# Kernel optimization log

Hardware: AMD Instinct MI355X
Metric: run time of the kernel (lower is better)

## Reference

```python
import jax, jax.numpy as jnp
import numpy as np

B, S, D = 32, 1024, 256
K, H, L = 64, 4, 4
KH, DV = K // H, D // H  # pooling key size per head, pooling value size
EPS = 1e-5
SCALE = 1.0 / np.sqrt(K).astype(np.float32)  # both encoder and pooling use sqrt(1/key_size)


def _ln(x, gamma=None, beta=None):
    m = jnp.mean(x, axis=-1, keepdims=True)
    v = jnp.mean(jnp.square(x - m), axis=-1, keepdims=True)
    y = (x - m) * jax.lax.rsqrt(v + EPS)
    if gamma is not None:
        y = y * gamma + beta
    return y


def setup_inputs() -> dict:
    key = jax.random.key(0)
    ks = iter(jax.random.split(key, 32))

    def w(shape, fan_in):
        return jax.random.normal(next(ks), shape, jnp.float32) / np.sqrt(fan_in).astype(np.float32)

    inp = {
        "input": jax.random.normal(next(ks), (B, S, D), jnp.float32),
        "lin0_W": w((D, D), D), "lin0_b": jnp.zeros((D,), jnp.float32),
        # stacked params for the 4 AttentionEncoder layers
        "enc_Wk": w((L, D, K), D), "enc_bk": jnp.zeros((L, K), jnp.float32),
        "enc_Wq": w((L, D, K), D), "enc_bq": jnp.zeros((L, K), jnp.float32),
        "enc_Wv": w((L, D, D), D), "enc_bv": jnp.zeros((L, D), jnp.float32),
        "enc_Wb": w((L, D, 1), D), "enc_bb": jnp.zeros((L, 1), jnp.float32),
        "enc_Wff": w((L, D, D), D), "enc_bff": jnp.zeros((L, D), jnp.float32),
        "enc_g1": jnp.ones((L, D), jnp.float32), "enc_beta1": jnp.zeros((L, D), jnp.float32),
        # multi-head pooling head
        "pool_Wk": w((D, KH), D), "pool_bk": jnp.zeros((KH,), jnp.float32),
        "pool_Wv": w((D, DV), D), "pool_bv": jnp.zeros((DV,), jnp.float32),
        "queries": jax.random.normal(next(ks), (H, KH), jnp.float32),
        "lin1_W": w((D, 2), D), "lin1_b": jnp.zeros((2,), jnp.float32),
    }
    return inp


def reference(input, lin0_W, lin0_b, enc_Wk, enc_bk, enc_Wq, enc_bq, enc_Wv, enc_bv,
              enc_Wb, enc_bb, enc_Wff, enc_bff, enc_g1, enc_beta1,
              pool_Wk, pool_bk, pool_Wv, pool_bv, queries, lin1_W, lin1_b):
    # NOTE: original code computes act0(lin0(input)) and then discards it (dead code);
    # it is omitted here since it does not affect the output.
    x = input
    for i in range(L):
        k = (x @ enc_Wk[i] + enc_bk[i]) * SCALE          # [B,S,K]
        q = x @ enc_Wq[i] + enc_bq[i]                     # [B,S,K]
        v = x @ enc_Wv[i] + enc_bv[i]                     # [B,S,D]
        bias = x @ enc_Wb[i] + enc_bb[i]                  # [B,S,1], broadcast over columns
        scores = jax.nn.sigmoid(jnp.einsum('bik,bjk->bij', k, q) + bias)  # [B,S,S]
        attn = jnp.einsum('bij,bjd->bid', scores, v)      # [B,S,D]
        res = _ln(x + attn, enc_g1[i], enc_beta1[i])
        ff = jax.nn.relu(res @ enc_Wff[i] + enc_bff[i])
        x = _ln(res + ff)                                 # norm2: no affine
    # multi-head pooling with learned queries
    pk = (x @ pool_Wk + pool_bk) * SCALE                  # [B,S,KH]
    pv = x @ pool_Wv + pool_bv                            # [B,S,DV]
    sc = jnp.einsum('bsk,hk->bsh', pk, queries)           # [B,S,H]
    sc = jax.nn.softmax(sc, axis=1)                       # softmax over sequence
    pooled = jnp.einsum('bsh,bsd->bhd', sc, pv).reshape(x.shape[0], -1)  # [B, H*DV]=[B,D]
    return pooled @ lin1_W + lin1_b                       # [B,2]
```

## Files before the change

### kernel.cpp

```cpp
#include <hip/hip_runtime.h>
#include <hip/hip_bf16.h>
#include <math.h>

#define BB 32
#define SS 1024
#define DD 256
#define MM (BB*SS)
#define LEPS 1e-5f

typedef __bf16 bf16x8 __attribute__((ext_vector_type(8)));
typedef __bf16 bf16x4 __attribute__((ext_vector_type(4)));
typedef float f32x4 __attribute__((ext_vector_type(4)));

__global__ __launch_bounds__(256) void cast_wt(const float* __restrict__ W,
                                               __bf16* __restrict__ WT,
                                               int N, float scale, int dstride, int noff) {
    int n = blockIdx.x, l = blockIdx.z, k = threadIdx.x;
    WT[(size_t)dstride * l + (size_t)(n + noff) * 256 + k] =
        (__bf16)(W[(size_t)256 * N * l + (size_t)k * N + n] * scale);
}

__global__ __launch_bounds__(128) void bias_combine(const float* __restrict__ bk,
                                                    const float* __restrict__ bq,
                                                    float* __restrict__ dst) {
    int l = blockIdx.x, j = threadIdx.x;
    dst[l * 128 + j] = (j < 64) ? bk[l * 64 + j] * 0.125f : bq[l * 64 + (j - 64)];
}

__global__ __launch_bounds__(256) void cast_x(const float* __restrict__ x, __bf16* __restrict__ xb) {
    size_t i = ((size_t)blockIdx.x * 256 + threadIdx.x) * 8;
    float4 a = *(const float4*)(x + i);
    float4 b = *(const float4*)(x + i + 4);
    __bf16 o[8] __attribute__((aligned(16)));
    o[0] = (__bf16)a.x; o[1] = (__bf16)a.y; o[2] = (__bf16)a.z; o[3] = (__bf16)a.w;
    o[4] = (__bf16)b.x; o[5] = (__bf16)b.y; o[6] = (__bf16)b.z; o[7] = (__bf16)b.w;
    *(bf16x8*)(xb + i) = *(bf16x8*)o;
}

template <int BN, int MODE>
__global__ __launch_bounds__(256) void gemm_mfma(const __bf16* __restrict__ A,
                                                 const __bf16* __restrict__ WT,
                                                 const float* __restrict__ bias,
                                                 float bscale, int relu,
                                                 void* __restrict__ Cv, void* __restrict__ Cv2,
                                                 int N) {
    constexpr int MR = (BN == 128) ? 4 : 2;
    constexpr int NC = (BN == 128) ? 4 : BN / 16;
    const int t = threadIdx.x;
    const int w = t >> 6, lane = t & 63;
    const int m0 = blockIdx.x * 128;
    const int n0 = blockIdx.y * BN;
    const size_t wt_z = (MODE == 3) ? (size_t)blockIdx.z * SS * 256 : 0;
    const size_t c_z  = (MODE == 3) ? (size_t)blockIdx.z * 256 * (size_t)N : 0;
    const int wr = (BN == 128) ? (w >> 1) * 64 : w * 32;
    const int wc = (BN == 128) ? (w & 1) * 64 : 0;
    __shared__ __align__(16) __bf16 smem[128 * 64 + BN * 64];
    __bf16 (*Al)[64] = (__bf16(*)[64])smem;
    __bf16 (*Wl)[64] = (__bf16(*)[64])(smem + 128 * 64);
    f32x4 acc[MR][NC] = {};

    for (int k0 = 0; k0 < 256; k0 += 64) {
        __syncthreads();
        {
            int r = t >> 1, half = t & 1;
            const __bf16* src = A + (size_t)(m0 + r) * 256 + k0 + half * 32;
            bf16x8 v0 = *(const bf16x8*)(src);
            bf16x8 v1 = *(const bf16x8*)(src + 8);
            bf16x8 v2 = *(const bf16x8*)(src + 16);
            bf16x8 v3 = *(const bf16x8*)(src + 24);
            int cb = half * 4;
            *(bf16x8*)&Al[r][((cb + 0) ^ (r & 7)) * 8] = v0;
            *(bf16x8*)&Al[r][((cb + 1) ^ (r & 7)) * 8] = v1;
            *(bf16x8*)&Al[r][((cb + 2) ^ (r & 7)) * 8] = v2;
            *(bf16x8*)&Al[r][((cb + 3) ^ (r & 7)) * 8] = v3;
        }
        if (BN == 128) {
            int r = t >> 1, half = t & 1;
            const __bf16* src = WT + wt_z + (size_t)(n0 + r) * 256 + k0 + half * 32;
            bf16x8 v0 = *(const bf16x8*)(src);
            bf16x8 v1 = *(const bf16x8*)(src + 8);
            bf16x8 v2 = *(const bf16x8*)(src + 16);
            bf16x8 v3 = *(const bf16x8*)(src + 24);
            int cb = half * 4;
            *(bf16x8*)&Wl[r][((cb + 0) ^ (r & 7)) * 8] = v0;
            *(bf16x8*)&Wl[r][((cb + 1) ^ (r & 7)) * 8] = v1;
            *(bf16x8*)&Wl[r][((cb + 2) ^ (r & 7)) * 8] = v2;
            *(bf16x8*)&Wl[r][((cb + 3) ^ (r & 7)) * 8] = v3;
        } else if (BN == 64) {
            int n = t >> 2, q = t & 3;
            const __bf16* src = WT + (size_t)(n0 + n) * 256 + k0 + q * 16;
            bf16x8 v0 = *(const bf16x8*)src;
            bf16x8 v1 = *(const bf16x8*)(src + 8);
            *(bf16x8*)&Wl[n][((q * 2 + 0) ^ (n & 7)) * 8] = v0;
            *(bf16x8*)&Wl[n][((q * 2 + 1) ^ (n & 7)) * 8] = v1;
        } else {
            if (t < 128) {
                int n = t >> 3, c = t & 7;
                bf16x8 v = *(const bf16x8*)(WT + (size_t)(n0 + n) * 256 + k0 + c * 8);
                *(bf16x8*)&Wl[n][(c ^ (n & 7)) * 8] = v;
            }
        }
        __syncthreads();
#pragma unroll
        for (int ks = 0; ks < 2; ks++) {
            int c = ks * 4 + (lane >> 4);
            bf16x8 af[MR];
#pragma unroll
            for (int mf = 0; mf < MR; mf++) {
                int i = wr + mf * 16 + (lane & 15);
                af[mf] = *(const bf16x8*)&Al[i][(c ^ (i & 7)) * 8];
            }
#pragma unroll
            for (int nf = 0; nf < NC; nf++) {
                int n = wc + nf * 16 + (lane & 15);
                bf16x8 bfr = *(const bf16x8*)&Wl[n][(c ^ (n & 7)) * 8];
#pragma unroll
                for (int mf = 0; mf < MR; mf++)
                    acc[mf][nf] = __builtin_amdgcn_mfma_f32_16x16x32_bf16(af[mf], bfr, acc[mf][nf], 0, 0, 0);
            }
        }
    }
    if (MODE == 3) {
        __syncthreads();
#pragma unroll
        for (int mf = 0; mf < MR; mf++) {
#pragma unroll
            for (int nf = 0; nf < NC; nf++) {
                int col = wc + nf * 16 + (lane & 15);
#pragma unroll
                for (int r = 0; r < 4; r++) {
                    int row = wr + mf * 16 + (lane >> 4) * 4 + r;
                    float v = acc[mf][nf][r] + bias[m0 + row];
                    smem[row * 128 + (((col >> 3) ^ (row & 15)) * 8) + (col & 7)] = (__bf16)v;
                }
            }
        }
        __syncthreads();
#pragma unroll
        for (int p = 0; p < 2; p++) {
            int row = p * 64 + (t >> 2);
            int cq = (t & 3) * 4;
            __bf16* dst = (__bf16*)Cv + c_z + (size_t)(m0 + row) * N + n0 + (t & 3) * 32;
#pragma unroll
            for (int u = 0; u < 4; u++) {
                int ch = (cq + u) ^ (row & 15);
                *(bf16x8*)(dst + u * 8) = *(const bf16x8*)&smem[row * 128 + ch * 8];
            }
        }
        return;
    }
#pragma unroll
    for (int mf = 0; mf < MR; mf++) {
#pragma unroll
        for (int nf = 0; nf < NC; nf++) {
            int col = n0 + wc + nf * 16 + (lane & 15);
            float bcol = bias[col] * bscale;
#pragma unroll
            for (int r = 0; r < 4; r++) {
                int row = m0 + wr + mf * 16 + (lane >> 4) * 4 + r;
                float v = acc[mf][nf][r] + bcol;
                if (relu) v = fmaxf(v, 0.f);
                if (MODE == 2) {
                    if (col < 64) ((__bf16*)Cv)[(size_t)row * 64 + col] = (__bf16)v;
                    else ((__bf16*)Cv2)[(size_t)row * 64 + (col - 64)] = (__bf16)v;
                } else if (MODE == 1) {
                    ((__bf16*)Cv)[(size_t)row * N + col] = (__bf16)v;
                } else {
                    ((float*)Cv)[(size_t)row * N + col] = v;
                }
            }
        }
    }
}

__global__ __launch_bounds__(256) void bias_gemv(const __bf16* __restrict__ X,
                                                 const float* __restrict__ Wb,
                                                 const float* __restrict__ bb,
                                                 float* __restrict__ out) {
    int wave = threadIdx.x >> 6, lane = threadIdx.x & 63;
    size_t row = (size_t)blockIdx.x * 4 + wave;
    bf16x4 xv = *(const bf16x4*)(X + row * 256 + lane * 4);
    float4 wv = *(const float4*)(Wb + lane * 4);
    float p = (float)xv[0] * wv.x + (float)xv[1] * wv.y + (float)xv[2] * wv.z + (float)xv[3] * wv.w;
    for (int off = 32; off; off >>= 1) p += __shfl_down(p, off, 64);
    if (lane == 0) out[row] = p + bb[0];
}

__global__ __launch_bounds__(512, 4) void attn_mfma(const __bf16* __restrict__ kb,
                                                    const __bf16* __restrict__ qb,
                                                    const __bf16* __restrict__ vT,
                                                    const float* __restrict__ biasb,
                                                    const __bf16* __restrict__ xinb,
                                                    const float* __restrict__ gamma,
                                                    const float* __restrict__ beta,
                                                    __bf16* __restrict__ outb) {
    int h = blockIdx.x;
    int blow = h & 7, rest = h >> 3;
    int ib = rest & 15;
    int b = blow + (rest >> 4) * 8;
    const int i0 = ib * 64;
    const int t = threadIdx.x;
    const int w = t >> 6, lane = t & 63;
    const int iq = w >> 1;
    const int dhalf = w & 1;

    __shared__ __align__(16) __bf16 Kl[64][64];
    __shared__ __align__(16) __bf16 Ql[64][64];
    __shared__ __align__(16) __bf16 Vl[256][64];
    __shared__ __align__(16) __bf16 Sl[64][64];
    __shared__ float bsh[64];
    __shared__ float rowred[2][64][2];

    const int qj = t >> 3, qc = t & 7;
    const __bf16* qsrc_base = qb + ((size_t)(b * SS + qj)) * 64 + qc * 8;
    const int vd = t >> 1, vjh = t & 1;
    const __bf16* vsrc_base = vT + ((size_t)b * 256 + vd) * SS + vjh * 32;

    {
        int i = t >> 3, c = t & 7;
        bf16x8 v = *(const bf16x8*)(kb + ((size_t)(b * SS + i0 + i)) * 64 + c * 8);
        *(bf16x8*)&Kl[i][(c ^ (i & 7)) * 8] = v;
        if (t < 64) bsh[t] = biasb[b * SS + i0 + t];
    }
    {
        bf16x8 qv = *(const bf16x8*)(qsrc_base);
        *(bf16x8*)&Ql[qj][(qc ^ (qj & 7)) * 8] = qv;
#pragma unroll
        for (int u = 0; u < 4; u++) {
            bf16x8 v = *(const bf16x8*)(vsrc_base + u * 8);
            *(bf16x8*)&Vl[vd][((vjh * 4 + u) ^ (vd & 7)) * 8] = v;
        }
    }
    __syncthreads();

    f32x4 acc[8] = {};

    for (int j0 = 0; j0 < SS; j0 += 64) {
        const bool has_next = (j0 + 64) < SS;
        bf16x8 qn;
        bf16x8 vn0, vn1, vn2, vn3;
        if (has_next) {
            qn = *(const bf16x8*)(qsrc_base + (size_t)(j0 + 64) * 64);
            const __bf16* vs = vsrc_base + j0 + 64;
            vn0 = *(const bf16x8*)(vs);
            vn1 = *(const bf16x8*)(vs + 8);
            vn2 = *(const bf16x8*)(vs + 16);
            vn3 = *(const bf16x8*)(vs + 24);
        }
#pragma unroll
        for (int jj = 0; jj < 2; jj++) {
            int jq = (w & 1) * 2 + jj;
            f32x4 sacc = {0.f, 0.f, 0.f, 0.f};
            __builtin_amdgcn_s_setprio(1);
#pragma unroll
            for (int ks = 0; ks < 2; ks++) {
                int i = iq * 16 + (lane & 15);
                int ck = ks * 4 + (lane >> 4);
                bf16x8 a = *(const bf16x8*)&Kl[i][(ck ^ (i & 7)) * 8];
                int j = jq * 16 + (lane & 15);
                bf16x8 bq = *(const bf16x8*)&Ql[j][(ck ^ (j & 7)) * 8];
                sacc = __builtin_amdgcn_mfma_f32_16x16x32_bf16(a, bq, sacc, 0, 0, 0);
            }
            __builtin_amdgcn_s_setprio(0);
            int jcol = jq * 16 + (lane & 15);
#pragma unroll
            for (int r = 0; r < 4; r++) {
                int irow = iq * 16 + (lane >> 4) * 4 + r;
                float x = sacc[r] + bsh[irow];
                float sg = 1.f / (1.f + __expf(-x));
                Sl[irow][(((jcol >> 3) ^ (irow & 7)) * 8) + (jcol & 7)] = (__bf16)sg;
            }
        }
        __syncthreads();
        bf16x8 am[2];
#pragma unroll
        for (int m = 0; m < 2; m++) {
            int i = iq * 16 + (lane & 15);
            int cj = m * 4 + (lane >> 4);
            am[m] = *(const bf16x8*)&Sl[i][(cj ^ (i & 7)) * 8];
        }
        __builtin_amdgcn_s_setprio(1);
#pragma unroll
        for (int dq = 0; dq < 8; dq++) {
            int d = dhalf * 128 + dq * 16 + (lane & 15);
#pragma unroll
            for (int m = 0; m < 2; m++) {
                int cj = m * 4 + (lane >> 4);
                bf16x8 bv = *(const bf16x8*)&Vl[d][(cj ^ (d & 7)) * 8];
                acc[dq] = __builtin_amdgcn_mfma_f32_16x16x32_bf16(am[m], bv, acc[dq], 0, 0, 0);
            }
        }
        __builtin_amdgcn_s_setprio(0);
        __syncthreads();
        if (has_next) {
            *(bf16x8*)&Ql[qj][(qc ^ (qj & 7)) * 8] = qn;
            *(bf16x8*)&Vl[vd][((vjh * 4 + 0) ^ (vd & 7)) * 8] = vn0;
            *(bf16x8*)&Vl[vd][((vjh * 4 + 1) ^ (vd & 7)) * 8] = vn1;
            *(bf16x8*)&Vl[vd][((vjh * 4 + 2) ^ (vd & 7)) * 8] = vn2;
            *(bf16x8*)&Vl[vd][((vjh * 4 + 3) ^ (vd & 7)) * 8] = vn3;
            __syncthreads();
        }
    }

#pragma unroll
    for (int r = 0; r < 4; r++) {
        int il = iq * 16 + (lane >> 4) * 4 + r;
        size_t rowoff = ((size_t)(b * SS + i0 + il)) * 256 + dhalf * 128 + (lane & 15);
#pragma unroll
        for (int dq = 0; dq < 8; dq++)
            acc[dq][r] += (float)xinb[rowoff + dq * 16];
    }
    float sr[4], qr[4];
#pragma unroll
    for (int r = 0; r < 4; r++) {
        float s = 0.f, q = 0.f;
#pragma unroll
        for (int dq = 0; dq < 8; dq++) {
            float v = acc[dq][r];
            s += v; q += v * v;
        }
#pragma unroll
        for (int mask = 8; mask; mask >>= 1) {
            s += __shfl_xor(s, mask, 64);
            q += __shfl_xor(q, mask, 64);
        }
        sr[r] = s; qr[r] = q;
    }
    if ((lane & 15) == 0) {
#pragma unroll
        for (int r = 0; r < 4; r++) {
            int il = iq * 16 + (lane >> 4) * 4 + r;
            rowred[dhalf][il][0] = sr[r];
            rowred[dhalf][il][1] = qr[r];
        }
    }
    __syncthreads();
    float gv[8], bv2[8];
#pragma unroll
    for (int dq = 0; dq < 8; dq++) {
        int d = dhalf * 128 + dq * 16 + (lane & 15);
        gv[dq] = gamma[d];
        bv2[dq] = beta[d];
    }
#pragma unroll
    for (int r = 0; r < 4; r++) {
        int il = iq * 16 + (lane >> 4) * 4 + r;
        float st = rowred[0][il][0] + rowred[1][il][0];
        float qt = rowred[0][il][1] + rowred[1][il][1];
        float mean = st * (1.f / 256.f);
        float var = qt * (1.f / 256.f) - mean * mean;
        float inv = 1.f / sqrtf(var + LEPS);
        size_t rowoff = ((size_t)(b * SS + i0 + il)) * 256 + dhalf * 128 + (lane & 15);
#pragma unroll
        for (int dq = 0; dq < 8; dq++) {
            float o = (acc[dq][r] - mean) * inv * gv[dq] + bv2[dq];
            outb[rowoff + dq * 16] = (__bf16)o;
        }
    }
}

__global__ __launch_bounds__(512) void gemm_ff_ln2(const __bf16* __restrict__ A,
                                                   const __bf16* __restrict__ WT,
                                                   const float* __restrict__ bias,
                                                   const __bf16* __restrict__ resid,
                                                   __bf16* __restrict__ outb) {
    const int t = threadIdx.x;
    const int w = t >> 6, lane = t & 63;
    const int m0 = blockIdx.x * 128;
    const int wr = (w >> 2) * 64, wc = (w & 3) * 64;
    __shared__ __align__(16) __bf16 Al[128][64];
    __shared__ __align__(16) __bf16 Wl[256][64];
    __shared__ float rowred[4][128][2];
    f32x4 acc[4][4] = {};

    for (int k0 = 0; k0 < 256; k0 += 64) {
        __syncthreads();
        {
            int r = t >> 2, c0 = (t & 3) * 2;
            const __bf16* src = A + (size_t)(m0 + r) * 256 + k0 + c0 * 8;
            bf16x8 v0 = *(const bf16x8*)src;
            bf16x8 v1 = *(const bf16x8*)(src + 8);
            *(bf16x8*)&Al[r][((c0 + 0) ^ (r & 7)) * 8] = v0;
            *(bf16x8*)&Al[r][((c0 + 1) ^ (r & 7)) * 8] = v1;
        }
        {
            int n = t >> 1, c0 = (t & 1) * 4;
            const __bf16* src = WT + (size_t)n * 256 + k0 + c0 * 8;
#pragma unroll
            for (int u = 0; u < 4; u++) {
                bf16x8 v = *(const bf16x8*)(src + u * 8);
                *(bf16x8*)&Wl[n][((c0 + u) ^ (n & 7)) * 8] = v;
            }
        }
        __syncthreads();
#pragma unroll
        for (int ks = 0; ks < 2; ks++) {
            int c = ks * 4 + (lane >> 4);
            bf16x8 af[4];
#pragma unroll
            for (int mf = 0; mf < 4; mf++) {
                int i = wr + mf * 16 + (lane & 15);
                af[mf] = *(const bf16x8*)&Al[i][(c ^ (i & 7)) * 8];
            }
#pragma unroll
            for (int nf = 0; nf < 4; nf++) {
                int n = wc + nf * 16 + (lane & 15);
                bf16x8 bfr = *(const bf16x8*)&Wl[n][(c ^ (n & 7)) * 8];
#pragma unroll
                for (int mf = 0; mf < 4; mf++)
                    acc[mf][nf] = __builtin_amdgcn_mfma_f32_16x16x32_bf16(af[mf], bfr, acc[mf][nf], 0, 0, 0);
            }
        }
    }
    float colb[4];
#pragma unroll
    for (int nf = 0; nf < 4; nf++) colb[nf] = bias[wc + nf * 16 + (lane & 15)];
#pragma unroll
    for (int mf = 0; mf < 4; mf++) {
#pragma unroll
        for (int r = 0; r < 4; r++) {
            int rl = wr + mf * 16 + (lane >> 4) * 4 + r;
            const __bf16* rrow = resid + (size_t)(m0 + rl) * 256 + wc + (lane & 15);
            float s = 0.f, q = 0.f;
#pragma unroll
            for (int nf = 0; nf < 4; nf++) {
                float v = fmaxf(acc[mf][nf][r] + colb[nf], 0.f) + (float)rrow[nf * 16];
                acc[mf][nf][r] = v;
                s += v; q += v * v;
            }
#pragma unroll
            for (int msk = 1; msk <= 8; msk <<= 1) {
                s += __shfl_xor(s, msk, 64);
                q += __shfl_xor(q, msk, 64);
            }
            if ((lane & 15) == 0) {
                rowred[w & 3][rl][0] = s;
                rowred[w & 3][rl][1] = q;
            }
        }
    }
    __syncthreads();
#pragma unroll
    for (int mf = 0; mf < 4; mf++) {
#pragma unroll
        for (int r = 0; r < 4; r++) {
            int rl = wr + mf * 16 + (lane >> 4) * 4 + r;
            float s = rowred[0][rl][0] + rowred[1][rl][0] + rowred[2][rl][0] + rowred[3][rl][0];
            float q = rowred[0][rl][1] + rowred[1][rl][1] + rowred[2][rl][1] + rowred[3][rl][1];
            float mean = s * (1.f / 256.f);
            float var = q * (1.f / 256.f) - mean * mean;
            float inv = 1.f / sqrtf(var + LEPS);
            size_t base = (size_t)(m0 + rl) * 256 + wc + (lane & 15);
#pragma unroll
            for (int nf = 0; nf < 4; nf++) {
                float o = (acc[mf][nf][r] - mean) * inv;
                outb[base + nf * 16] = (__bf16)o;
            }
        }
    }
}

__global__ __launch_bounds__(256) void pool_softmax(const float* __restrict__ pk,
                                                    const float* __restrict__ queries,
                                                    float* __restrict__ wout) {
    const int b = blockIdx.x, h = blockIdx.y;
    const int t = threadIdx.x;
    const int wv = t >> 6, lane = t & 63;
    __shared__ float qv[16];
    __shared__ float redm[4], reds[4];
    if (t < 16) qv[t] = queries[h * 16 + t];
    __syncthreads();
    float sc[4];
#pragma unroll
    for (int c = 0; c < 4; c++) {
        int s = c * 256 + t;
        const float* p = pk + ((size_t)b * SS + s) * 16;
        float4 a0 = *(const float4*)p;
        float4 a1 = *(const float4*)(p + 4);
        float4 a2 = *(const float4*)(p + 8);
        float4 a3 = *(const float4*)(p + 12);
        sc[c] = a0.x * qv[0] + a0.y * qv[1] + a0.z * qv[2] + a0.w * qv[3]
              + a1.x * qv[4] + a1.y * qv[5] + a1.z * qv[6] + a1.w * qv[7]
              + a2.x * qv[8] + a2.y * qv[9] + a2.z * qv[10] + a2.w * qv[11]
              + a3.x * qv[12] + a3.y * qv[13] + a3.z * qv[14] + a3.w * qv[15];
    }
    float m = fmaxf(fmaxf(sc[0], sc[1]), fmaxf(sc[2], sc[3]));
    for (int off = 32; off; off >>= 1) m = fmaxf(m, __shfl_xor(m, off, 64));
    if (lane == 0) redm[wv] = m;
    __syncthreads();
    m = fmaxf(fmaxf(redm[0], redm[1]), fmaxf(redm[2], redm[3]));
    float e[4];
    float sum = 0.f;
#pragma unroll
    for (int c = 0; c < 4; c++) { e[c] = expf(sc[c] - m); sum += e[c]; }
    for (int off = 32; off; off >>= 1) sum += __shfl_xor(sum, off, 64);
    if (lane == 0) reds[wv] = sum;
    __syncthreads();
    float inv = 1.f / (reds[0] + reds[1] + reds[2] + reds[3]);
#pragma unroll
    for (int c = 0; c < 4; c++)
        wout[((size_t)(b * 4 + h)) * SS + c * 256 + t] = e[c] * inv;
}

__global__ __launch_bounds__(256) void pool_wsum(const float* __restrict__ wgt,
                                                 const float* __restrict__ pv,
                                                 float* __restrict__ partial) {
    const int b = blockIdx.x, c = blockIdx.y;
    const int h = threadIdx.x >> 6, d = threadIdx.x & 63;
    const float* wrow = wgt + ((size_t)(b * 4 + h)) * SS + c * 64;
    const float* pvb = pv + ((size_t)(b * SS + c * 64)) * 64 + d;
    float a = 0.f;
#pragma unroll 8
    for (int s = 0; s < 64; s++) a += wrow[s] * pvb[(size_t)s * 64];
    partial[((size_t)b * 16 + c) * 256 + threadIdx.x] = a;
}

__global__ __launch_bounds__(256) void pool_final(const float* __restrict__ partial,
                                                  const float* __restrict__ W1,
                                                  const float* __restrict__ b1,
                                                  float* __restrict__ out) {
    const int b = blockIdx.x, t = threadIdx.x;
    __shared__ float r0[256], r1[256];
    float a = 0.f;
#pragma unroll
    for (int c = 0; c < 16; c++) a += partial[((size_t)b * 16 + c) * 256 + t];
    r0[t] = a * W1[t * 2 + 0];
    r1[t] = a * W1[t * 2 + 1];
    __syncthreads();
    for (int off = 128; off > 0; off >>= 1) {
        if (t < off) { r0[t] += r0[t + off]; r1[t] += r1[t + off]; }
        __syncthreads();
    }
    if (t == 0) {
        out[b * 2 + 0] = r0[0] + b1[0];
        out[b * 2 + 1] = r1[0] + b1[1];
    }
}

extern "C" void kernel_launch(void* const* d_in, const int* in_sizes, int n_in,
                              void* d_out, int out_size, void* d_ws, size_t ws_size,
                              hipStream_t stream) {
    const float* input = (const float*)d_in[0];
    const float* eWk = (const float*)d_in[3];
    const float* ebk = (const float*)d_in[4];
    const float* eWq = (const float*)d_in[5];
    const float* ebq = (const float*)d_in[6];
    const float* eWv = (const float*)d_in[7];
    const float* ebv = (const float*)d_in[8];
    const float* eWb = (const float*)d_in[9];
    const float* ebb = (const float*)d_in[10];
    const float* eWff = (const float*)d_in[11];
    const float* ebff = (const float*)d_in[12];
    const float* eg1 = (const float*)d_in[13];
    const float* ebe1 = (const float*)d_in[14];
    const float* pWk = (const float*)d_in[15];
    const float* pbk = (const float*)d_in[16];
    const float* pWv = (const float*)d_in[17];
    const float* pbv = (const float*)d_in[18];
    const float* qrs = (const float*)d_in[19];
    const float* W1 = (const float*)d_in[20];
    const float* b1 = (const float*)d_in[21];
    float* out = (float*)d_out;

    float* ws = (float*)d_ws;
    float* xbuf = ws;
    __bf16* xbf = (__bf16*)(xbuf + (size_t)MM * DD);
    float* tmp2 = (float*)(xbf + (size_t)MM * DD);
    float* r3 = tmp2 + (size_t)MM * DD;
    __bf16* tmp2bf = (__bf16*)r3;
    __bf16* vTb = tmp2bf + (size_t)MM * DD;
    float* r4 = r3 + (size_t)MM * DD;
    __bf16* kbf = (__bf16*)r4;
    __bf16* qbf = kbf + (size_t)MM * 64;
    float* bbuf = r4 + (size_t)MM * (DD / 2);
    __bf16* wbf = (__bf16*)(bbuf + MM);

    __bf16* WkqT = wbf;
    __bf16* WvT = WkqT + 4 * 128 * 256;
    __bf16* WffT = WvT + 4 * 256 * 256;
    __bf16* pWkT = WffT + 4 * 256 * 256;
    __bf16* pWvT = pWkT + 16 * 256;
    float* biasc = (float*)(pWvT + 64 * 256);

    float* pkbuf = tmp2;
    float* pvbuf = tmp2 + (size_t)MM * 16;
    float* wgtbuf = tmp2 + (size_t)MM * 80;
    float* partial = wgtbuf + (size_t)BB * 4 * SS;

    const float SC = 0.125f;

    cast_wt<<<dim3(64, 1, 4), 256, 0, stream>>>(eWk, WkqT, 64, SC, 128 * 256, 0);
    cast_wt<<<dim3(64, 1, 4), 256, 0, stream>>>(eWq, WkqT, 64, 1.f, 128 * 256, 64);
    cast_wt<<<dim3(256, 1, 4), 256, 0, stream>>>(eWv, WvT, 256, 1.f, 256 * 256, 0);
    cast_wt<<<dim3(256, 1, 4), 256, 0, stream>>>(eWff, WffT, 256, 1.f, 256 * 256, 0);
    cast_wt<<<dim3(16, 1, 1), 256, 0, stream>>>(pWk, pWkT, 16, SC, 16 * 256, 0);
    cast_wt<<<dim3(64, 1, 1), 256, 0, stream>>>(pWv, pWvT, 64, 1.f, 64 * 256, 0);
    bias_combine<<<4, 128, 0, stream>>>(ebk, ebq, biasc);
    cast_x<<<MM * DD / (256 * 8), 256, 0, stream>>>(input, xbf);

    for (int l = 0; l < 4; l++) {
        gemm_mfma<128, 2><<<dim3(MM / 128, 1), 256, 0, stream>>>(
            xbf, WkqT + (size_t)l * 128 * 256, biasc + l * 128, 1.f, 0, kbf, qbf, 64);
        gemm_mfma<128, 3><<<dim3(2, SS / 128, BB), 256, 0, stream>>>(
            WvT + (size_t)l * 256 * 256, xbf, ebv + l * DD, 1.f, 0, vTb, nullptr, SS);
        bias_gemv<<<MM / 4, 256, 0, stream>>>(xbf, eWb + (size_t)l * DD, ebb + l, bbuf);
        attn_mfma<<<dim3(512, 1), 512, 0, stream>>>(kbf, qbf, vTb, bbuf, xbf,
                                                    eg1 + l * DD, ebe1 + l * DD, tmp2bf);
        gemm_ff_ln2<<<dim3(MM / 128, 1), 512, 0, stream>>>(
            tmp2bf, WffT + (size_t)l * 256 * 256, ebff + l * DD, tmp2bf, xbf);
    }
    gemm_mfma<16, 0><<<dim3(MM / 128, 1), 256, 0, stream>>>(xbf, pWkT, pbk, SC, 0, pkbuf, nullptr, 16);
    gemm_mfma<64, 0><<<dim3(MM / 128, 1), 256, 0, stream>>>(xbf, pWvT, pbv, 1.f, 0, pvbuf, nullptr, 64);
    pool_softmax<<<dim3(BB, 4), 256, 0, stream>>>(pkbuf, qrs, wgtbuf);
    pool_wsum<<<dim3(BB, 16), 256, 0, stream>>>(wgtbuf, pvbuf, partial);
    pool_final<<<BB, 256, 0, stream>>>(partial, W1, b1, out);
}
```

Baseline: 441.0 us.

## Load V fragments directly from global and keep K and bias in registers

The attention kernel stops staging K, V and the bias in shared memory. Each lane now keeps its K MFMA fragments and bias values in registers, and reads V fragments straight from global memory inside the PV loop. The next Q tile is written to shared memory right after the score barrier, which drops one barrier per iteration. This cuts LDS use and synchronisation, which may allow more blocks per CU, but V is now read redundantly by the four waves sharing a d-half and is no longer prefetched, so global load latency is exposed.

```diff
diff --git a/kernel.cpp b/kernel.cpp
--- a/kernel.cpp
+++ b/kernel.cpp
@@ -204,32 +204,25 @@
     const int iq = w >> 1;
     const int dhalf = w & 1;
 
-    __shared__ __align__(16) __bf16 Kl[64][64];
     __shared__ __align__(16) __bf16 Ql[64][64];
-    __shared__ __align__(16) __bf16 Vl[256][64];
     __shared__ __align__(16) __bf16 Sl[64][64];
-    __shared__ float bsh[64];
     __shared__ float rowred[2][64][2];
+
+    bf16x8 kf[2];
+    {
+        const __bf16* kr = kb + ((size_t)(b * SS + i0 + iq * 16 + (lane & 15))) * 64 + (lane >> 4) * 8;
+        kf[0] = *(const bf16x8*)(kr);
+        kf[1] = *(const bf16x8*)(kr + 32);
+    }
+    float4 biasr = *(const float4*)(biasb + (size_t)b * SS + i0 + iq * 16 + (lane >> 4) * 4);
+
+    const __bf16* vbase = vT + ((size_t)b * 256 + dhalf * 128 + (lane & 15)) * SS + (lane >> 4) * 8;
 
     const int qj = t >> 3, qc = t & 7;
     const __bf16* qsrc_base = qb + ((size_t)(b * SS + qj)) * 64 + qc * 8;
-    const int vd = t >> 1, vjh = t & 1;
-    const __bf16* vsrc_base = vT + ((size_t)b * 256 + vd) * SS + vjh * 32;
-
-    {
-        int i = t >> 3, c = t & 7;
-        bf16x8 v = *(const bf16x8*)(kb + ((size_t)(b * SS + i0 + i)) * 64 + c * 8);
-        *(bf16x8*)&Kl[i][(c ^ (i & 7)) * 8] = v;
-        if (t < 64) bsh[t] = biasb[b * SS + i0 + t];
-    }
     {
         bf16x8 qv = *(const bf16x8*)(qsrc_base);
         *(bf16x8*)&Ql[qj][(qc ^ (qj & 7)) * 8] = qv;
-#pragma unroll
-        for (int u = 0; u < 4; u++) {
-            bf16x8 v = *(const bf16x8*)(vsrc_base + u * 8);
-            *(bf16x8*)&Vl[vd][((vjh * 4 + u) ^ (vd & 7)) * 8] = v;
-        }
     }
     __syncthreads();
 
@@ -238,15 +231,7 @@
     for (int j0 = 0; j0 < SS; j0 += 64) {
         const bool has_next = (j0 + 64) < SS;
         bf16x8 qn;
-        bf16x8 vn0, vn1, vn2, vn3;
-        if (has_next) {
-            qn = *(const bf16x8*)(qsrc_base + (size_t)(j0 + 64) * 64);
-            const __bf16* vs = vsrc_base + j0 + 64;
-            vn0 = *(const bf16x8*)(vs);
-            vn1 = *(const bf16x8*)(vs + 8);
-            vn2 = *(const bf16x8*)(vs + 16);
-            vn3 = *(const bf16x8*)(vs + 24);
-        }
+        if (has_next) qn = *(const bf16x8*)(qsrc_base + (size_t)(j0 + 64) * 64);
 #pragma unroll
         for (int jj = 0; jj < 2; jj++) {
             int jq = (w & 1) * 2 + jj;
@@ -254,24 +239,23 @@
             __builtin_amdgcn_s_setprio(1);
 #pragma unroll
             for (int ks = 0; ks < 2; ks++) {
-                int i = iq * 16 + (lane & 15);
+                int j = jq * 16 + (lane & 15);
                 int ck = ks * 4 + (lane >> 4);
-                bf16x8 a = *(const bf16x8*)&Kl[i][(ck ^ (i & 7)) * 8];
-                int j = jq * 16 + (lane & 15);
                 bf16x8 bq = *(const bf16x8*)&Ql[j][(ck ^ (j & 7)) * 8];
-                sacc = __builtin_amdgcn_mfma_f32_16x16x32_bf16(a, bq, sacc, 0, 0, 0);
+                sacc = __builtin_amdgcn_mfma_f32_16x16x32_bf16(kf[ks], bq, sacc, 0, 0, 0);
             }
             __builtin_amdgcn_s_setprio(0);
             int jcol = jq * 16 + (lane & 15);
 #pragma unroll
             for (int r = 0; r < 4; r++) {
                 int irow = iq * 16 + (lane >> 4) * 4 + r;
-                float x = sacc[r] + bsh[irow];
+                float x = sacc[r] + biasr[r];
                 float sg = 1.f / (1.f + __expf(-x));
                 Sl[irow][(((jcol >> 3) ^ (irow & 7)) * 8) + (jcol & 7)] = (__bf16)sg;
             }
         }
         __syncthreads();
+        if (has_next) *(bf16x8*)&Ql[qj][(qc ^ (qj & 7)) * 8] = qn;
         bf16x8 am[2];
 #pragma unroll
         for (int m = 0; m < 2; m++) {
@@ -279,27 +263,17 @@
             int cj = m * 4 + (lane >> 4);
             am[m] = *(const bf16x8*)&Sl[i][(cj ^ (i & 7)) * 8];
         }
-        __builtin_amdgcn_s_setprio(1);
 #pragma unroll
         for (int dq = 0; dq < 8; dq++) {
-            int d = dhalf * 128 + dq * 16 + (lane & 15);
-#pragma unroll
-            for (int m = 0; m < 2; m++) {
-                int cj = m * 4 + (lane >> 4);
-                bf16x8 bv = *(const bf16x8*)&Vl[d][(cj ^ (d & 7)) * 8];
-                acc[dq] = __builtin_amdgcn_mfma_f32_16x16x32_bf16(am[m], bv, acc[dq], 0, 0, 0);
-            }
-        }
-        __builtin_amdgcn_s_setprio(0);
-        __syncthreads();
-        if (has_next) {
-            *(bf16x8*)&Ql[qj][(qc ^ (qj & 7)) * 8] = qn;
-            *(bf16x8*)&Vl[vd][((vjh * 4 + 0) ^ (vd & 7)) * 8] = vn0;
-            *(bf16x8*)&Vl[vd][((vjh * 4 + 1) ^ (vd & 7)) * 8] = vn1;
-            *(bf16x8*)&Vl[vd][((vjh * 4 + 2) ^ (vd & 7)) * 8] = vn2;
-            *(bf16x8*)&Vl[vd][((vjh * 4 + 3) ^ (vd & 7)) * 8] = vn3;
-            __syncthreads();
-        }
+            const __bf16* vp = vbase + (size_t)dq * 16 * SS + j0;
+            bf16x8 bv0 = *(const bf16x8*)(vp);
+            bf16x8 bv1 = *(const bf16x8*)(vp + 32);
+            __builtin_amdgcn_s_setprio(1);
+            acc[dq] = __builtin_amdgcn_mfma_f32_16x16x32_bf16(am[0], bv0, acc[dq], 0, 0, 0);
+            acc[dq] = __builtin_amdgcn_mfma_f32_16x16x32_bf16(am[1], bv1, acc[dq], 0, 0, 0);
+            __builtin_amdgcn_s_setprio(0);
+        }
+        __syncthreads();
     }
 
 #pragma unroll
```

After: 798.3 us. +81.0%, slower.
